# Optimization experiments

Measured on AMD Instinct MI355X. Metric: run time of the kernel, lower is better.

## Reference

```python
import jax, jax.numpy as jnp
import numpy as np

T, B, D, H, HH, OUT = 512, 128, 256, 1024, 256, 128
EPS = 1e-3

def _ln(x, gamma, beta):
    # layer_norm over feature dim, eps=0.001, matching torch reciprocal(sqrt(var+eps))
    m = jnp.mean(x, -1, keepdims=True)
    xs = x - m
    v = jnp.mean(xs * xs, -1, keepdims=True)
    return gamma * xs * jax.lax.rsqrt(v + EPS) + beta

def _ln_all(h, base, units, gamma, beta):
    # normalize each of `base` gate blocks independently over `units`
    b = h.shape[0]
    hr = h.reshape(b, base, units)
    m = jnp.mean(hr, -1, keepdims=True)
    xs = hr - m
    v = jnp.mean(xs * xs, -1, keepdims=True)
    hn = (xs * jax.lax.rsqrt(v + EPS)).reshape(b, base * units)
    return gamma * hn + beta

def setup_inputs() -> dict:
    key = jax.random.key(0)
    ks = jax.random.split(key, 12)
    return {
        "x": jax.random.normal(ks[0], (T, B, D), jnp.float32),
        "Wx": jax.random.normal(ks[1], (4 * H, D), jnp.float32) * (1.0 / np.sqrt(D)),
        "Wh": jax.random.normal(ks[2], (4 * H, H), jnp.float32) * (1.0 / np.sqrt(H)),
        "bias": jax.random.normal(ks[3], (4 * H,), jnp.float32) * 0.1,
        "lna_gamma": jnp.ones((4 * H,), jnp.float32),
        "lna_beta": jnp.zeros((4 * H,), jnp.float32),
        "ln_gamma": jnp.ones((H,), jnp.float32),
        "ln_beta": jnp.zeros((H,), jnp.float32),
        "zb": jax.random.normal(ks[4], (4, HH, HH), jnp.float32) * 0.01,   # ib/jb/fb/ob _zb
        "zbeta": jax.random.normal(ks[5], (4, HH, H), jnp.float32) * 0.01, # ib/jb/fb/ob _beta
        "zw_w": jax.random.normal(ks[6], (8, HH, HH), jnp.float32) * 0.01, # ix,jx,fx,ox,ih,jh,fh,oh _zw_w
        "zw_b": jnp.ones((8, HH), jnp.float32),
        "alpha": jnp.full((8, HH, H), 0.1 / HH, jnp.float32) + jax.random.normal(ks[7], (8, HH, H), jnp.float32) * 1e-4,
        "hyp_Wx": jax.random.normal(ks[8], (4 * HH, D + H), jnp.float32) * (1.0 / np.sqrt(D + H)),
        "hyp_bx": jnp.zeros((4 * HH,), jnp.float32),
        "hyp_Wh": jax.random.normal(ks[9], (4 * HH, HH), jnp.float32) * (1.0 / np.sqrt(HH)),
        "hyp_bh": jnp.zeros((4 * HH,), jnp.float32),
        "hyp_lna_gamma": jnp.ones((4 * HH,), jnp.float32),
        "hyp_lna_beta": jnp.zeros((4 * HH,), jnp.float32),
        "hyp_ln_gamma": jnp.ones((HH,), jnp.float32),
        "hyp_ln_beta": jnp.zeros((HH,), jnp.float32),
        "fc_W": jax.random.normal(ks[10], (OUT, H), jnp.float32) * (1.0 / np.sqrt(H)),
        "fc_b": jnp.zeros((OUT,), jnp.float32),
    }

def reference(x, Wx, Wh, bias, lna_gamma, lna_beta, ln_gamma, ln_beta, zb, zbeta,
              zw_w, zw_b, alpha, hyp_Wx, hyp_bx, hyp_Wh, hyp_bh,
              hyp_lna_gamma, hyp_lna_beta, hyp_ln_gamma, hyp_ln_beta, fc_W, fc_b):
    b4 = bias.reshape(4, H)

    def step(carry, xt):
        h, c, hh, ch = carry  # main (B,H), hyper (B,HH)
        # ---- hypernetwork LSTM cell (layer-norm LSTM) ----
        g = jnp.concatenate([xt, h], 1) @ hyp_Wx.T + hyp_bx + hh @ hyp_Wh.T + hyp_bh
        g = _ln_all(g, 4, HH, hyp_lna_gamma, hyp_lna_beta)
        hi, hf, hg, ho = jnp.split(g, 4, 1)  # ingate, forgetgate, cellgate, outgate
        ch_n = jax.nn.sigmoid(hf) * ch + jax.nn.sigmoid(hi) * jnp.tanh(hg)
        hyp = jax.nn.sigmoid(ho) * jnp.tanh(_ln(ch_n, hyp_ln_gamma, hyp_ln_beta))
        # ---- hyper-modulation: per-gate scale vectors and bias adjustments ----
        z = jnp.einsum('bq,kqp->kbp', hyp, zw_w) + zw_b[:, None, :]   # (8,B,HH)
        sc = jnp.einsum('kbp,kph->kbh', z, alpha)                     # (8,B,H)
        bz = jnp.einsum('bq,kqp->kbp', hyp, zb)                       # (4,B,HH)
        badj = jnp.einsum('kbp,kph->kbh', bz, zbeta)                  # (4,B,H)
        # ---- main LSTM gates (order i, j, f, o) ----
        xg = (xt @ Wx.T).reshape(B, 4, H).transpose(1, 0, 2)          # (4,B,H)
        hg2 = (h @ Wh.T).reshape(B, 4, H).transpose(1, 0, 2)          # (4,B,H)
        gates = sc[:4] * xg + sc[4:] * hg2 + b4[:, None, :] + badj    # (4,B,H)
        gates = _ln_all(gates.transpose(1, 0, 2).reshape(B, 4 * H), 4, H, lna_gamma, lna_beta)
        i, j, f, o = jnp.split(gates, 4, 1)
        c_n = jax.nn.sigmoid(f) * c + jax.nn.sigmoid(i) * jnp.tanh(j)
        h_n = jax.nn.sigmoid(o) * jnp.tanh(_ln(c_n, ln_gamma, ln_beta))
        return (h_n, c_n, hyp, ch_n), None

    init = (jnp.zeros((B, H), x.dtype), jnp.zeros((B, H), x.dtype),
            jnp.zeros((B, HH), x.dtype), jnp.zeros((B, HH), x.dtype))
    (h_f, _, _, _), _ = jax.lax.scan(step, init, x)
    return h_f @ fc_W.T + fc_b  # (B, OUT)
```

## Files before the change

### kernel.cpp

```cpp
#include <hip/hip_runtime.h>
#include <math.h>

#define T_STEPS 512
#define BATCH   128
#define DIN     256
#define HMAIN   1024
#define HHYP    256
#define OUTN    128
#define EPS     1e-3f

#define KSPLIT_NONE (1<<30)
#define NBLK 512

typedef __attribute__((ext_vector_type(4))) float f32x4;
typedef __attribute__((ext_vector_type(8))) short s16x8;

__device__ __forceinline__ float sigm(float x){ return 1.f/(1.f + expf(-x)); }

__device__ __forceinline__ unsigned short f2bf(float f){
    union { float f; unsigned u; } x; x.f = f;
    unsigned r = x.u + 0x7FFFu + ((x.u >> 16) & 1u);
    return (unsigned short)(r >> 16);
}

__device__ __forceinline__ float agf(const float* p){
    return __hip_atomic_load(const_cast<float*>(p), __ATOMIC_RELAXED, __HIP_MEMORY_SCOPE_AGENT);
}
__device__ __forceinline__ unsigned long long agu8(const void* p){
    return __hip_atomic_load(const_cast<unsigned long long*>((const unsigned long long*)p),
                             __ATOMIC_RELAXED, __HIP_MEMORY_SCOPE_AGENT);
}
__device__ __forceinline__ void agsf(float* p, float v){
    __hip_atomic_store(p, v, __ATOMIC_RELAXED, __HIP_MEMORY_SCOPE_AGENT);
}
__device__ __forceinline__ void agsu(unsigned* p, unsigned v){
    __hip_atomic_store(p, v, __ATOMIC_RELAXED, __HIP_MEMORY_SCOPE_AGENT);
}

__device__ __forceinline__ void gbar(unsigned* cnt, unsigned phase, int bid, int tid){
    __syncthreads();
    if (tid < 16){
        if (tid == (bid & 15))
            __hip_atomic_fetch_add(&cnt[tid*32], 1u, __ATOMIC_RELAXED, __HIP_MEMORY_SCOPE_AGENT);
        const unsigned tg = phase * (NBLK/16);
        while (__hip_atomic_load(&cnt[tid*32], __ATOMIC_RELAXED, __HIP_MEMORY_SCOPE_AGENT) < tg)
            __builtin_amdgcn_s_sleep(4);
    }
    __syncthreads();
}

#define BM 32
#define BN 64
#define KT 32
__device__ void gemm_dev(const float* __restrict__ A1, int lda1, int ksplit,
                         const float* __restrict__ A2, int lda2,
                         const float* __restrict__ Bp, int ldb, int b_nk,
                         const float* __restrict__ bias,
                         float* __restrict__ C, int ldc,
                         int K, int k0, int mtile, int ntile)
{
    __shared__ __align__(16) float As[KT][BM+4];
    __shared__ __align__(16) float Bs[KT][BN+4];
    const int tid = threadIdx.x;
    const int mt = tid >> 4, nt = tid & 15;
    const int m0g = mtile*BM, n0g = ntile*BN;
    float acc[4][4];
    #pragma unroll
    for (int i=0;i<4;++i) { acc[i][0]=0;acc[i][1]=0;acc[i][2]=0;acc[i][3]=0; }
    for (int kt = 0; kt < K; kt += KT) {
        __syncthreads();
        #pragma unroll
        for (int i=0;i<8;++i){
            int e = tid + i*128;
            int m = e >> 5, k = e & 31;
            int gk = k0 + kt + k, gm = m0g + m;
            float v = (gk < ksplit) ? A1[(size_t)gm*lda1 + gk]
                                    : A2[(size_t)gm*lda2 + (gk - ksplit)];
            As[k][m] = v;
        }
        if (b_nk) {
            #pragma unroll
            for (int i=0;i<16;++i){
                int e = tid + i*128;
                int n = e >> 5, k = e & 31;
                Bs[k][n] = Bp[(size_t)(n0g + n)*ldb + (k0 + kt + k)];
            }
        } else {
            #pragma unroll
            for (int i=0;i<16;++i){
                int e = tid + i*128;
                int k = e >> 6, n = e & 63;
                Bs[k][n] = Bp[(size_t)(k0 + kt + k)*ldb + (n0g + n)];
            }
        }
        __syncthreads();
        #pragma unroll
        for (int k=0;k<KT;++k){
            float4 av = *(const float4*)(&As[k][4*mt]);
            float4 bv = *(const float4*)(&Bs[k][4*nt]);
            acc[0][0]+=av.x*bv.x; acc[0][1]+=av.x*bv.y; acc[0][2]+=av.x*bv.z; acc[0][3]+=av.x*bv.w;
            acc[1][0]+=av.y*bv.x; acc[1][1]+=av.y*bv.y; acc[1][2]+=av.y*bv.z; acc[1][3]+=av.y*bv.w;
            acc[2][0]+=av.z*bv.x; acc[2][1]+=av.z*bv.y; acc[2][2]+=av.z*bv.z; acc[2][3]+=av.z*bv.w;
            acc[3][0]+=av.w*bv.x; acc[3][1]+=av.w*bv.y; acc[3][2]+=av.w*bv.z; acc[3][3]+=av.w*bv.w;
        }
    }
    #pragma unroll
    for (int i=0;i<4;++i){
        int gm = m0g + 4*mt + i;
        #pragma unroll
        for (int j=0;j<4;++j){
            int gn = n0g + 4*nt + j;
            float v = acc[i][j];
            if (bias) v += bias[gn];
            C[(size_t)gm*ldc + gn] = v;
        }
    }
}

#define ASTR 40
__device__ void gemm_mfma(const float* __restrict__ A1, int lda1, int ksplit,
                          const float* __restrict__ A2, int lda2,
                          const unsigned short* __restrict__ B, int ldb,
                          const float* __restrict__ bias,
                          float* __restrict__ C, int ldc,
                          int K, int k0, int mtile, int ntile)
{
    __shared__ __align__(16) unsigned short As[32*ASTR];
    __shared__ __align__(16) unsigned short Bs[128*ASTR];
    const int tid = threadIdx.x;
    const int lane = tid & 63, w = tid >> 6;
    const int wm = (w >> 1) * 16, wn = (w & 1) * 64;
    const int fr = lane & 15, koff = (lane >> 4) * 8;
    const int m0g = mtile*32, n0g = ntile*128;

    f32x4 acc[4];
    #pragma unroll
    for (int j=0;j<4;++j) acc[j] = (f32x4){0.f,0.f,0.f,0.f};

    const int arow = tid >> 3, akc = (tid & 7) * 4;
    for (int kt = 0; kt < K; kt += 32) {
        __syncthreads();
        {
            int gk = k0 + kt + akc;
            int gm = m0g + arow;
            const float* src = (gk < ksplit) ? (A1 + (size_t)gm*lda1 + gk)
                                             : (A2 + (size_t)gm*lda2 + (gk - ksplit));
            float4 v = *(const float4*)src;
            unsigned short* d = &As[arow*ASTR + akc];
            d[0] = f2bf(v.x); d[1] = f2bf(v.y); d[2] = f2bf(v.z); d[3] = f2bf(v.w);
        }
        #pragma unroll
        for (int i=0;i<4;++i){
            int e = tid + i*256;
            int n = e >> 3, kc = (e & 7) * 4;
            ushort4 bv = *(const ushort4*)(B + (size_t)(n0g + n)*ldb + (k0 + kt + kc));
            unsigned short* d = &Bs[n*ASTR + kc];
            d[0] = bv.x; d[1] = bv.y; d[2] = bv.z; d[3] = bv.w;
        }
        __syncthreads();
        s16x8 af = *(const s16x8*)&As[(wm + fr)*ASTR + koff];
        #pragma unroll
        for (int j=0;j<4;++j){
            s16x8 bf = *(const s16x8*)&Bs[(wn + j*16 + fr)*ASTR + koff];
            acc[j] = __builtin_amdgcn_mfma_f32_16x16x32_bf16(af, bf, acc[j], 0, 0, 0);
        }
    }
    #pragma unroll
    for (int j=0;j<4;++j){
        int gn = n0g + wn + j*16 + fr;
        float bb = bias ? bias[gn] : 0.f;
        #pragma unroll
        for (int r=0;r<4;++r){
            int gm = m0g + wm + (lane >> 4)*4 + r;
            C[(size_t)gm*ldc + gn] = acc[j][r] + bb;
        }
    }
}

#define WSTR 264
template<int NF, int AMODE>
__device__ __forceinline__ void gemm_ws(
    const void* __restrict__ Aptr, int lda,
    const unsigned short* wtile,
    const float* __restrict__ bias,
    float* __restrict__ Cout, int ldc,
    int lane, int w)
{
    const int fr = lane & 15, kq = lane >> 4;
    f32x4 acc[2][NF];
    #pragma unroll
    for (int mf=0; mf<2; ++mf)
        #pragma unroll
        for (int nf=0; nf<NF; ++nf) acc[mf][nf] = (f32x4){0.f,0.f,0.f,0.f};
    const int r0 = w*32 + fr;
    #pragma unroll
    for (int kt=0; kt<256; kt+=32) {
        const int k = kt + kq*8;
        s16x8 a[2];
        #pragma unroll
        for (int mf=0; mf<2; ++mf) {
            const int row = r0 + mf*16;
            if (AMODE == 0) {
                const float* s = (const float*)Aptr + (size_t)row*lda + k;
                float4 v0 = *(const float4*)s;
                float4 v1 = *(const float4*)(s+4);
                union { s16x8 v; unsigned short u[8]; } tc;
                tc.u[0]=f2bf(v0.x); tc.u[1]=f2bf(v0.y); tc.u[2]=f2bf(v0.z); tc.u[3]=f2bf(v0.w);
                tc.u[4]=f2bf(v1.x); tc.u[5]=f2bf(v1.y); tc.u[6]=f2bf(v1.z); tc.u[7]=f2bf(v1.w);
                a[mf] = tc.v;
            } else {
                const unsigned short* s = (const unsigned short*)Aptr + (size_t)row*lda + k;
                union { unsigned long long q[2]; s16x8 v; } tc;
                tc.q[0] = agu8(s);
                tc.q[1] = agu8(s + 4);
                a[mf] = tc.v;
            }
        }
        #pragma unroll
        for (int nf=0; nf<NF; ++nf) {
            s16x8 b = *(const s16x8*)&wtile[(nf*16+fr)*WSTR + k];
            acc[0][nf] = __builtin_amdgcn_mfma_f32_16x16x32_bf16(a[0], b, acc[0][nf], 0,0,0);
            acc[1][nf] = __builtin_amdgcn_mfma_f32_16x16x32_bf16(a[1], b, acc[1][nf], 0,0,0);
        }
    }
    #pragma unroll
    for (int nf=0; nf<NF; ++nf) {
        const int col = nf*16 + fr;
        const float bb = bias ? bias[col] : 0.f;
        #pragma unroll
        for (int mf=0; mf<2; ++mf) {
            const int row = w*32 + mf*16 + kq*4;
            #pragma unroll
            for (int r=0; r<4; ++r)
                agsf(&Cout[(size_t)(row+r)*ldc + col], acc[mf][nf][r] + bb);
        }
    }
}

__device__ __forceinline__ void load_wtile(const unsigned short* __restrict__ src,
                                           int ld, unsigned short* dst, int rows, int tid)
{
    const int chunks = rows * 32;
    for (int cidx = tid; cidx < chunks; cidx += 256) {
        const int r = cidx >> 5, k8 = (cidx & 31) << 3;
        *(uint4*)&dst[r*WSTR + k8] = *(const uint4*)&src[(size_t)r*ld + k8];
    }
}

__global__ __launch_bounds__(256) void k_prep_convert(
    const float* __restrict__ hyp_Wx, const float* __restrict__ hyp_Wh,
    const float* __restrict__ hyp_bx, const float* __restrict__ hyp_bh,
    const float* __restrict__ Wx, const float* __restrict__ Wh,
    unsigned short* __restrict__ wcat1bf, unsigned short* __restrict__ wxbf,
    unsigned short* __restrict__ whbf, float* __restrict__ bias1,
    float* __restrict__ act1f, float* __restrict__ c, float* __restrict__ ch,
    unsigned int* __restrict__ act1bf_zero, unsigned int* __restrict__ gcnt_zero)
{
    size_t i = (size_t)blockIdx.x*256 + threadIdx.x;
    if (i < 1572864u) {
        int n = (int)(i / 1536), k = (int)(i % 1536);
        float v = (k < 1280) ? hyp_Wx[(size_t)n*1280 + k] : hyp_Wh[(size_t)n*256 + (k-1280)];
        wcat1bf[i] = f2bf(v); return;
    }
    i -= 1572864u;
    if (i < 1048576u) { wxbf[i] = f2bf(Wx[i]); return; }
    i -= 1048576u;
    if (i < 4194304u) { whbf[i] = f2bf(Wh[i]); return; }
    i -= 4194304u;
    if (i < 1024u) { bias1[i] = hyp_bx[i] + hyp_bh[i]; return; }
    i -= 1024u;
    if (i < 163840u) { act1f[i] = 0.f; return; }
    i -= 163840u;
    if (i < 131072u) { c[i] = 0.f; return; }
    i -= 131072u;
    if (i < 32768u) { ch[i] = 0.f; return; }
    i -= 32768u;
    if (i < 81920u) { act1bf_zero[i] = 0u; return; }
    i -= 81920u;
    if (i < 512u) { gcnt_zero[i] = 0u; return; }
}
#define PREP_TOTAL 7226880u

__global__ __launch_bounds__(128) void k_prep_wcomb(
    const float* __restrict__ zw_w, const float* __restrict__ zb,
    const float* __restrict__ alpha, const float* __restrict__ zbeta,
    float* __restrict__ wcombf32)
{
    int kk = blockIdx.z;
    const float* A = (kk < 8) ? (zw_w + (size_t)kk*65536) : (zb + (size_t)(kk-8)*65536);
    const float* Bm = (kk < 8) ? (alpha + (size_t)kk*262144) : (zbeta + (size_t)(kk-8)*262144);
    gemm_dev(A, 256, KSPLIT_NONE, A, 256, Bm, 1024, 0, nullptr,
             wcombf32 + (size_t)kk*262144, 1024, 256, 0, blockIdx.x, blockIdx.y);
}

__global__ __launch_bounds__(256) void k_prep_cvtcomb(
    const float* __restrict__ wcombf32, unsigned short* __restrict__ wcombbf)
{
    size_t i = (size_t)blockIdx.x*256 + threadIdx.x;
    if (i >= 3145728u) return;
    int kk = (int)(i / 262144u);
    int r  = (int)(i % 262144u);
    int n = r / 256, k = r % 256;
    wcombbf[i] = f2bf(wcombf32[(size_t)kk*262144 + (size_t)k*1024 + n]);
}

__global__ __launch_bounds__(256) void k_prep_bcomb(
    const float* __restrict__ zw_b, const float* __restrict__ alpha,
    float* __restrict__ bcomb)
{
    int k = blockIdx.x;
    int n = blockIdx.y*256 + threadIdx.x;
    float s = 0.f;
    for (int p=0;p<256;++p)
        s += zw_b[k*256+p] * alpha[(size_t)k*262144 + (size_t)p*1024 + n];
    bcomb[(size_t)k*1024 + n] = s;
}

__device__ __forceinline__ void breduce2(float& a, float& b, volatile float* buf, int tid){
    #pragma unroll
    for (int off = 32; off > 0; off >>= 1) { a += __shfl_xor(a, off); b += __shfl_xor(b, off); }
    __syncthreads();
    if ((tid & 63) == 0) { buf[(tid>>6)*2] = a; buf[(tid>>6)*2+1] = b; }
    __syncthreads();
    a = buf[0] + buf[2] + buf[4] + buf[6];
    b = buf[1] + buf[3] + buf[5] + buf[7];
}

__device__ __forceinline__ void hyper_cell6(
    int b, int tid, volatile float* cbuf,
    const float* __restrict__ gpart, const float* __restrict__ bias1,
    const float* __restrict__ lna_g, const float* __restrict__ lna_b,
    const float* __restrict__ ln_g, const float* __restrict__ ln_b,
    float* __restrict__ ch, unsigned short* __restrict__ act1bf)
{
    float v[4];
    #pragma unroll
    for (int g=0; g<4; ++g){
        size_t idx = (size_t)b*1024 + g*256 + tid;
        v[g] = agf(&gpart[idx]) + agf(&gpart[131072+idx]) + agf(&gpart[262144+idx])
             + agf(&gpart[393216+idx]) + agf(&gpart[524288+idx]) + agf(&gpart[655360+idx])
             + bias1[g*256 + tid];
    }
    #pragma unroll
    for (int g=0; g<4; ++g){
        float s = v[g], ss = v[g]*v[g];
        breduce2(s, ss, cbuf, tid);
        float m = s * (1.f/256.f);
        float var = ss * (1.f/256.f) - m*m;
        v[g] = (v[g]-m)*rsqrtf(var + EPS)*lna_g[g*256+tid] + lna_b[g*256+tid];
    }
    float chp = ch[b*256 + tid];
    float cn = sigm(v[1])*chp + sigm(v[0])*tanhf(v[2]);
    float s = cn, ss = cn*cn;
    breduce2(s, ss, cbuf, tid);
    float m = s*(1.f/256.f);
    float var = ss*(1.f/256.f) - m*m;
    float hn = sigm(v[3]) * tanhf((cn-m)*rsqrtf(var + EPS)*ln_g[tid] + ln_b[tid]);
    ch[b*256 + tid] = cn;
    unsigned hb = f2bf(hn);
    unsigned other = __shfl_down(hb, 1);
    if (!(tid & 1))
        agsu((unsigned*)(act1bf + (size_t)b*1280 + 1024 + tid), hb | (other << 16));
}

__device__ __forceinline__ void main_cell2(
    int b, int tid, volatile float* cbuf,
    const float* __restrict__ bias4,
    const float* __restrict__ lna_g, const float* __restrict__ lna_b,
    const float* __restrict__ ln_g, const float* __restrict__ ln_b,
    const float* __restrict__ xgbuf, const float* __restrict__ hgpart,
    const float* __restrict__ scb,
    float* __restrict__ c, unsigned short* __restrict__ act1bf,
    float* __restrict__ hfc)
{
    float gn[4][4];
    #pragma unroll
    for (int k=0;k<4;++k){
        float pre[4]; float s=0.f, ss=0.f;
        #pragma unroll
        for (int j=0;j<4;++j){
            int h = j*256 + tid;
            int n = k*1024 + h;
            size_t bh = (size_t)b*1024 + h;
            size_t bn = (size_t)b*4096 + n;
            float xgv = agf(&xgbuf[bn]);
            float hgv = agf(&hgpart[bn]) + agf(&hgpart[524288+bn])
                      + agf(&hgpart[1048576+bn]) + agf(&hgpart[1572864+bn]);
            float p = agf(&scb[(size_t)k*131072 + bh])*xgv
                    + agf(&scb[(size_t)(4+k)*131072 + bh])*hgv
                    + bias4[n] + agf(&scb[(size_t)(8+k)*131072 + bh]);
            pre[j] = p; s += p; ss += p*p;
        }
        breduce2(s, ss, cbuf, tid);
        float m = s*(1.f/1024.f);
        float var = ss*(1.f/1024.f) - m*m;
        float rs = rsqrtf(var + EPS);
        #pragma unroll
        for (int j=0;j<4;++j){
            int h=j*256+tid, n=k*1024+h;
            gn[k][j] = (pre[j]-m)*rs*lna_g[n] + lna_b[n];
        }
    }
    float cnv[4]; float s=0.f, ss=0.f;
    #pragma unroll
    for (int j=0;j<4;++j){
        int h=j*256+tid;
        float cv = c[(size_t)b*1024+h];
        float x = sigm(gn[2][j])*cv + sigm(gn[0][j])*tanhf(gn[1][j]);
        cnv[j]=x; s+=x; ss+=x*x;
    }
    breduce2(s, ss, cbuf, tid);
    float m=s*(1.f/1024.f);
    float var=ss*(1.f/1024.f)-m*m;
    float rs=rsqrtf(var + EPS);
    #pragma unroll
    for (int j=0;j<4;++j){
        int h=j*256+tid;
        float hv = sigm(gn[3][j])*tanhf((cnv[j]-m)*rs*ln_g[h] + ln_b[h]);
        c[(size_t)b*1024+h] = cnv[j];
        hfc[(size_t)b*1024 + h] = hv;
        unsigned hb = f2bf(hv);
        unsigned other = __shfl_down(hb, 1);
        if (!(tid & 1))
            agsu((unsigned*)(act1bf + (size_t)b*1280 + h), hb | (other << 16));
    }
}

__device__ __forceinline__ void hyper_cell_body(
    const float* __restrict__ lna_g, const float* __restrict__ lna_b,
    const float* __restrict__ ln_g, const float* __restrict__ ln_b,
    const float* __restrict__ gpart, const float* __restrict__ bias1,
    float* __restrict__ ch, float* __restrict__ act1, int b, int tid)
{
    __shared__ float buf[8];
    float v[4];
    #pragma unroll
    for (int g=0; g<4; ++g){
        int idx = b*1024 + g*256 + tid;
        v[g] = gpart[idx] + gpart[131072 + idx] + gpart[262144 + idx] + gpart[393216 + idx]
             + bias1[g*256 + tid];
    }
    #pragma unroll
    for (int g=0; g<4; ++g){
        float s = v[g], ss = v[g]*v[g];
        breduce2(s, ss, buf, tid);
        float m = s * (1.f/256.f);
        float var = ss * (1.f/256.f) - m*m;
        v[g] = (v[g]-m)*rsqrtf(var + EPS)*lna_g[g*256+tid] + lna_b[g*256+tid];
    }
    float chp = ch[b*256 + tid];
    float cn = sigm(v[1])*chp + sigm(v[0])*tanhf(v[2]);
    float s = cn, ss = cn*cn;
    breduce2(s, ss, buf, tid);
    float m = s*(1.f/256.f);
    float var = ss*(1.f/256.f) - m*m;
    float hn = sigm(v[3]) * tanhf((cn-m)*rsqrtf(var + EPS)*ln_g[tid] + ln_b[tid]);
    ch[b*256 + tid] = cn;
    act1[b*1280 + 1024 + tid] = hn;
}

__device__ __forceinline__ void main_cell_body(
    const float* __restrict__ bias4,
    const float* __restrict__ lna_g, const float* __restrict__ lna_b,
    const float* __restrict__ ln_g, const float* __restrict__ ln_b,
    const float* __restrict__ xghg, const float* __restrict__ scb,
    float* __restrict__ c, float* __restrict__ act1, int b, int tid)
{
    __shared__ float buf[8];
    float gn[4][4];
    #pragma unroll
    for (int k=0;k<4;++k){
        float pre[4]; float s=0.f, ss=0.f;
        #pragma unroll
        for (int j=0;j<4;++j){
            int h = j*256 + tid;
            int n = k*1024 + h;
            int bh = b*1024 + h;
            float xgv = xghg[b*4096 + n];
            float hgv = xghg[524288 + b*4096 + n];
            float p = scb[k*131072 + bh]*xgv + scb[(4+k)*131072 + bh]*hgv
                    + bias4[n] + scb[(8+k)*131072 + bh];
            pre[j] = p; s += p; ss += p*p;
        }
        breduce2(s, ss, buf, tid);
        float m = s*(1.f/1024.f);
        float var = ss*(1.f/1024.f) - m*m;
        float rs = rsqrtf(var + EPS);
        #pragma unroll
        for (int j=0;j<4;++j){
            int h=j*256+tid, n=k*1024+h;
            gn[k][j] = (pre[j]-m)*rs*lna_g[n] + lna_b[n];
        }
    }
    float cnv[4]; float s=0.f, ss=0.f;
    #pragma unroll
    for (int j=0;j<4;++j){
        int h=j*256+tid;
        float cv = c[b*1024+h];
        float x = sigm(gn[2][j])*cv + sigm(gn[0][j])*tanhf(gn[1][j]);
        cnv[j]=x; s+=x; ss+=x*x;
    }
    breduce2(s, ss, buf, tid);
    float m=s*(1.f/1024.f);
    float var=ss*(1.f/1024.f)-m*m;
    float rs=rsqrtf(var + EPS);
    #pragma unroll
    for (int j=0;j<4;++j){
        int h=j*256+tid;
        float hv = sigm(gn[3][j])*tanhf((cnv[j]-m)*rs*ln_g[h] + ln_b[h]);
        c[b*1024+h] = cnv[j];
        act1[b*1280 + h] = hv;
    }
}

__global__ __launch_bounds__(256) void k_step1(
    const float* __restrict__ xt, const float* __restrict__ act1,
    const unsigned short* __restrict__ wcat1bf,
    const unsigned short* __restrict__ wxbf, const unsigned short* __restrict__ whbf,
    float* __restrict__ gpart, float* __restrict__ xghg)
{
    int bid = blockIdx.x;
    if (bid < 128) {
        int sp = bid >> 5, r = bid & 31;
        gemm_mfma(xt, 256, 256, act1, 1280, wcat1bf, 1536, nullptr,
                  gpart + (size_t)sp*131072, 1024, 384, sp*384, r >> 3, r & 7);
    } else if (bid < 256) {
        int r = bid - 128;
        gemm_mfma(xt, 256, KSPLIT_NONE, xt, 256, wxbf, 256, nullptr,
                  xghg, 4096, 256, 0, r >> 5, r & 31);
    } else {
        int r = bid - 256;
        gemm_mfma(act1, 1280, KSPLIT_NONE, act1, 1280, whbf, 1024, nullptr,
                  xghg + 524288, 4096, 1024, 0, r >> 5, r & 31);
    }
}

__global__ __launch_bounds__(256) void k_step2(
    const float* __restrict__ act1, const unsigned short* __restrict__ wcombbf,
    const float* __restrict__ bcomb, float* __restrict__ scb)
{
    int bid = blockIdx.x;
    int kk = bid >> 5, r = bid & 31;
    const float* bias = (kk < 8) ? (bcomb + (size_t)kk*1024) : nullptr;
    gemm_mfma(act1 + 1024, 1280, KSPLIT_NONE, act1 + 1024, 1280,
              wcombbf + (size_t)kk*262144, 256, bias,
              scb + (size_t)kk*131072, 1024, 256, 0, r >> 3, r & 7);
}

__global__ __launch_bounds__(256) void k_hyper_cell(
    const float* __restrict__ lna_g, const float* __restrict__ lna_b,
    const float* __restrict__ ln_g, const float* __restrict__ ln_b,
    const float* __restrict__ gpart, const float* __restrict__ bias1,
    float* __restrict__ ch, float* __restrict__ act1)
{
    hyper_cell_body(lna_g, lna_b, ln_g, ln_b, gpart, bias1, ch, act1,
                    blockIdx.x, threadIdx.x);
}

__global__ __launch_bounds__(256) void k_main_cell(
    const float* __restrict__ bias4,
    const float* __restrict__ lna_g, const float* __restrict__ lna_b,
    const float* __restrict__ ln_g, const float* __restrict__ ln_b,
    const float* __restrict__ xghg, const float* __restrict__ scb,
    float* __restrict__ c, float* __restrict__ act1)
{
    main_cell_body(bias4, lna_g, lna_b, ln_g, ln_b, xghg, scb, c, act1,
                   blockIdx.x, threadIdx.x);
}

__global__ __launch_bounds__(256, 2) void k_persist4(
    const float* __restrict__ x,
    const unsigned short* __restrict__ wcat1bf,
    const unsigned short* __restrict__ wxbf,
    const unsigned short* __restrict__ whbf,
    const unsigned short* __restrict__ wcombbf,
    const float* __restrict__ bcomb, const float* __restrict__ bias1,
    const float* __restrict__ bias4,
    const float* __restrict__ lna_g, const float* __restrict__ lna_b,
    const float* __restrict__ ln_g, const float* __restrict__ ln_b,
    const float* __restrict__ hlna_g, const float* __restrict__ hlna_b,
    const float* __restrict__ hln_g, const float* __restrict__ hln_b,
    float* __restrict__ gpart, float* __restrict__ hgpart,
    float* __restrict__ xgbuf, float* __restrict__ scb,
    unsigned short* __restrict__ act1bf, float* __restrict__ hfc,
    float* __restrict__ c, float* __restrict__ ch,
    unsigned* __restrict__ gcnt)
{
    const int bid = blockIdx.x, tid = threadIdx.x;
    const int lane = tid & 63, w = tid >> 6;
    __shared__ __align__(16) unsigned short wlds[25344];
    __shared__ float cbuf[8];

    if (bid < 96) {
        load_wtile(wcat1bf + (size_t)((bid & 15)*64)*1536 + (bid >> 4)*256,
                   1536, wlds, 64, tid);
    } else if (bid < 352) {
        int h_ = bid - 96;
        load_wtile(whbf + (size_t)((h_ >> 2)*64)*1024 + (h_ & 3)*256,
                   1024, wlds, 64, tid);
    } else if (bid < 416) {
        load_wtile(wxbf + (size_t)(bid - 352)*64*256, 256, wlds, 64, tid);
    }
    if (bid < 384) {
        int kk = bid >> 5, mt = bid & 31;
        load_wtile(wcombbf + (size_t)kk*262144 + (size_t)(mt*32)*256,
                   256, wlds + 16896, 32, tid);
    }
    __syncthreads();

    unsigned phase = 0;
    for (int t = 0; t < T_STEPS; ++t) {
        const float* xt = x + (size_t)t*BATCH*DIN;

        if (bid < 96) {
            int nt = bid & 15, sp = bid >> 4;
            float* outp = gpart + (size_t)sp*131072 + nt*64;
            if (sp == 0)
                gemm_ws<4,0>(xt, 256, wlds, nullptr, outp, 1024, lane, w);
            else
                gemm_ws<4,2>(act1bf + (sp-1)*256, 1280, wlds, nullptr, outp, 1024, lane, w);
        }
        gbar(gcnt, ++phase, bid, tid);

        if (bid >= 96 && bid < 352) {
            int h_ = bid - 96, nt = h_ >> 2, sp = h_ & 3;
            gemm_ws<4,2>(act1bf + sp*256, 1280, wlds, nullptr,
                         hgpart + (size_t)sp*524288 + nt*64, 4096, lane, w);
        } else if (bid >= 352 && bid < 416) {
            gemm_ws<4,0>(xt, 256, wlds, nullptr,
                         xgbuf + (bid - 352)*64, 4096, lane, w);
        } else {
            int row = (bid >= 416) ? (bid - 416) : (bid < 32 ? 96 + bid : -1);
            if (row >= 0)
                hyper_cell6(row, tid, cbuf, gpart, bias1,
                            hlna_g, hlna_b, hln_g, hln_b, ch, act1bf);
        }
        gbar(gcnt, ++phase, bid, tid);

        if (bid < 384) {
            int kk = bid >> 5, mt = bid & 31;
            const float* bp = (kk < 8) ? (bcomb + (size_t)kk*1024 + mt*32) : nullptr;
            gemm_ws<2,2>(act1bf + 1024, 1280, wlds + 16896, bp,
                         scb + (size_t)kk*131072 + mt*32, 1024, lane, w);
        }
        gbar(gcnt, ++phase, bid, tid);

        if (bid < 128)
            main_cell2(bid, tid, cbuf, bias4, lna_g, lna_b, ln_g, ln_b,
                       xgbuf, hgpart, scb, c, act1bf, hfc);
        gbar(gcnt, ++phase, bid, tid);
    }
}

__global__ __launch_bounds__(128) void k_fc2(
    const float* __restrict__ fcW, const float* __restrict__ fcb,
    const float* __restrict__ hsrc, int ldh, float* __restrict__ out)
{
    int b = blockIdx.x, o = threadIdx.x;
    const float* h = hsrc + (size_t)b*ldh;
    float s = fcb[o];
    for (int k=0;k<1024;++k) s += h[k]*fcW[(size_t)o*1024 + k];
    out[b*OUTN + o] = s;
}

extern "C" void kernel_launch(void* const* d_in, const int* in_sizes, int n_in,
                              void* d_out, int out_size, void* d_ws, size_t ws_size,
                              hipStream_t stream)
{
    const float* x        = (const float*)d_in[0];
    const float* Wx       = (const float*)d_in[1];
    const float* Wh       = (const float*)d_in[2];
    const float* bias     = (const float*)d_in[3];
    const float* lna_g    = (const float*)d_in[4];
    const float* lna_b    = (const float*)d_in[5];
    const float* ln_g     = (const float*)d_in[6];
    const float* ln_b     = (const float*)d_in[7];
    const float* zb       = (const float*)d_in[8];
    const float* zbeta    = (const float*)d_in[9];
    const float* zw_w     = (const float*)d_in[10];
    const float* zw_b     = (const float*)d_in[11];
    const float* alpha    = (const float*)d_in[12];
    const float* hyp_Wx   = (const float*)d_in[13];
    const float* hyp_bx   = (const float*)d_in[14];
    const float* hyp_Wh   = (const float*)d_in[15];
    const float* hyp_bh   = (const float*)d_in[16];
    const float* hlna_g   = (const float*)d_in[17];
    const float* hlna_b   = (const float*)d_in[18];
    const float* hln_g    = (const float*)d_in[19];
    const float* hln_b    = (const float*)d_in[20];
    const float* fcW      = (const float*)d_in[21];
    const float* fcb      = (const float*)d_in[22];
    float* out = (float*)d_out;

    unsigned short* wcat1bf = (unsigned short*)d_ws;
    unsigned short* wxbf    = wcat1bf + 1572864;
    unsigned short* whbf    = wxbf + 1048576;
    unsigned short* wcombbf = whbf + 4194304;
    unsigned short* act1bf  = wcombbf + 3145728;
    float* fbase = (float*)(act1bf + 163840);
    float* bcomb = fbase;
    float* bias1 = bcomb + 8192;
    float* hfc   = bias1 + 1024;
    float* c     = hfc + 131072;
    float* ch    = c + 131072;
    float* act1o = ch + 32768;
    float* gpart = act1o + 163840;
    float* hgpart= gpart + 786432;
    float* xgbuf = hgpart + 2097152;
    float* scb   = xgbuf + 524288;
    unsigned* gcnt = (unsigned*)(scb + 1572864);
    float* wcombf32 = gpart;

    k_prep_convert<<<(PREP_TOTAL + 255)/256, 256, 0, stream>>>(
        hyp_Wx, hyp_Wh, hyp_bx, hyp_bh, Wx, Wh,
        wcat1bf, wxbf, whbf, bias1, act1o, c, ch,
        (unsigned int*)act1bf, gcnt);
    k_prep_wcomb<<<dim3(8,16,12), 128, 0, stream>>>(zw_w, zb, alpha, zbeta, wcombf32);
    k_prep_bcomb<<<dim3(8,4), 256, 0, stream>>>(zw_b, alpha, bcomb);
    k_prep_cvtcomb<<<(3145728 + 255)/256, 256, 0, stream>>>(wcombf32, wcombbf);

    static int use_pers = -1;
    if (use_pers < 0) {
        use_pers = 0;
        int dev = 0;
        if (hipGetDevice(&dev) == hipSuccess) {
            hipDeviceProp_t prop;
            if (hipGetDeviceProperties(&prop, dev) == hipSuccess) {
                int occ = 0;
                if (hipOccupancyMaxActiveBlocksPerMultiprocessor(
                        &occ, (const void*)k_persist4, 256, 0) == hipSuccess &&
                    occ >= 2 && occ * prop.multiProcessorCount >= NBLK) {
                    use_pers = 1;
                }
            }
        }
    }

    if (use_pers) {
        k_persist4<<<NBLK, 256, 0, stream>>>(
            x, wcat1bf, wxbf, whbf, wcombbf,
            bcomb, bias1, bias,
            lna_g, lna_b, ln_g, ln_b,
            hlna_g, hlna_b, hln_g, hln_b,
            gpart, hgpart, xgbuf, scb,
            act1bf, hfc, c, ch, gcnt);
        k_fc2<<<BATCH, 128, 0, stream>>>(fcW, fcb, hfc, 1024, out);
        return;
    }

    float* xghg = hgpart;
    for (int t = 0; t < T_STEPS; ++t) {
        const float* xt = x + (size_t)t*BATCH*DIN;
        k_step1<<<384, 256, 0, stream>>>(xt, act1o, wcat1bf, wxbf, whbf, gpart, xghg);
        k_hyper_cell<<<BATCH, 256, 0, stream>>>(hlna_g, hlna_b, hln_g, hln_b,
                                                gpart, bias1, ch, act1o);
        k_step2<<<384, 256, 0, stream>>>(act1o, wcombbf, bcomb, scb);
        k_main_cell<<<BATCH, 256, 0, stream>>>(bias, lna_g, lna_b, ln_g, ln_b,
                                               xghg, scb, c, act1o);
    }
    k_fc2<<<BATCH, 128, 0, stream>>>(fcW, fcb, act1o, 1280, out);
}
```

Measured before the change: 34.07 ms.

## Use a master-broadcast grid barrier and run hgpart/xg GEMMs in the first phase

Replaces the distributed 16-counter grid barrier with a two-level scheme. Every block increments a sharded counter, block 0 waits for all shards, then publishes the phase in a single flag that all other blocks poll with one thread. The Wh-hidden and Wx-input GEMMs now run in the same phase as the hyper-GEMM, so the phase with the hyper cell only does the hyper cell. The aim is to cut polling contention and barrier latency, and to shorten the critical path of each timestep. The cost is an extra hop through block 0 at every barrier, plus a bigger counter buffer to zero.

Measured after the change: 34.15 ms. Within noise of the previous version (+0.2%).

```diff
diff --git a/kernel.cpp b/kernel.cpp
--- a/kernel.cpp
+++ b/kernel.cpp
@@ -36,15 +36,29 @@
 __device__ __forceinline__ void agsu(unsigned* p, unsigned v){
     __hip_atomic_store(p, v, __ATOMIC_RELAXED, __HIP_MEMORY_SCOPE_AGENT);
 }
+__device__ __forceinline__ unsigned aglu(const unsigned* p){
+    return __hip_atomic_load(const_cast<unsigned*>(p), __ATOMIC_RELAXED, __HIP_MEMORY_SCOPE_AGENT);
+}
 
 __device__ __forceinline__ void gbar(unsigned* cnt, unsigned phase, int bid, int tid){
     __syncthreads();
-    if (tid < 16){
-        if (tid == (bid & 15))
-            __hip_atomic_fetch_add(&cnt[tid*32], 1u, __ATOMIC_RELAXED, __HIP_MEMORY_SCOPE_AGENT);
-        const unsigned tg = phase * (NBLK/16);
-        while (__hip_atomic_load(&cnt[tid*32], __ATOMIC_RELAXED, __HIP_MEMORY_SCOPE_AGENT) < tg)
-            __builtin_amdgcn_s_sleep(4);
+    if (bid == 0) {
+        if (tid < 16) {
+            if (tid == 0)
+                __hip_atomic_fetch_add(&cnt[0], 1u, __ATOMIC_RELAXED, __HIP_MEMORY_SCOPE_AGENT);
+            const unsigned tg = phase * (NBLK/16);
+            while (aglu(&cnt[tid*32]) < tg)
+                __builtin_amdgcn_s_sleep(1);
+        }
+        __syncthreads();
+        if (tid == 0)
+            agsu(&cnt[512], phase);
+    } else {
+        if (tid == 0) {
+            __hip_atomic_fetch_add(&cnt[(bid & 15)*32], 1u, __ATOMIC_RELAXED, __HIP_MEMORY_SCOPE_AGENT);
+            while (aglu(&cnt[512]) < phase)
+                __builtin_amdgcn_s_sleep(4);
+        }
     }
     __syncthreads();
 }
@@ -277,9 +291,9 @@
     i -= 32768u;
     if (i < 81920u) { act1bf_zero[i] = 0u; return; }
     i -= 81920u;
-    if (i < 512u) { gcnt_zero[i] = 0u; return; }
-}
-#define PREP_TOTAL 7226880u
+    if (i < 1024u) { gcnt_zero[i] = 0u; return; }
+}
+#define PREP_TOTAL 7227392u
 
 __global__ __launch_bounds__(128) void k_prep_wcomb(
     const float* __restrict__ zw_w, const float* __restrict__ zb,
@@ -568,7 +582,7 @@
                    blockIdx.x, threadIdx.x);
 }
 
-__global__ __launch_bounds__(256, 2) void k_persist4(
+__global__ __launch_bounds__(256, 2) void k_persist5(
     const float* __restrict__ x,
     const unsigned short* __restrict__ wcat1bf,
     const unsigned short* __restrict__ wxbf,
@@ -619,17 +633,17 @@
                 gemm_ws<4,0>(xt, 256, wlds, nullptr, outp, 1024, lane, w);
             else
                 gemm_ws<4,2>(act1bf + (sp-1)*256, 1280, wlds, nullptr, outp, 1024, lane, w);
-        }
-        gbar(gcnt, ++phase, bid, tid);
-
-        if (bid >= 96 && bid < 352) {
+        } else if (bid < 352) {
             int h_ = bid - 96, nt = h_ >> 2, sp = h_ & 3;
             gemm_ws<4,2>(act1bf + sp*256, 1280, wlds, nullptr,
                          hgpart + (size_t)sp*524288 + nt*64, 4096, lane, w);
-        } else if (bid >= 352 && bid < 416) {
+        } else if (bid < 416) {
             gemm_ws<4,0>(xt, 256, wlds, nullptr,
                          xgbuf + (bid - 352)*64, 4096, lane, w);
-        } else {
+        }
+        gbar(gcnt, ++phase, bid, tid);
+
+        {
             int row = (bid >= 416) ? (bid - 416) : (bid < 32 ? 96 + bid : -1);
             if (row >= 0)
                 hyper_cell6(row, tid, cbuf, gpart, bias1,
@@ -728,7 +742,7 @@
             if (hipGetDeviceProperties(&prop, dev) == hipSuccess) {
                 int occ = 0;
                 if (hipOccupancyMaxActiveBlocksPerMultiprocessor(
-                        &occ, (const void*)k_persist4, 256, 0) == hipSuccess &&
+                        &occ, (const void*)k_persist5, 256, 0) == hipSuccess &&
                     occ >= 2 && occ * prop.multiProcessorCount >= NBLK) {
                     use_pers = 1;
                 }
@@ -737,7 +751,7 @@
     }
 
     if (use_pers) {
-        k_persist4<<<NBLK, 256, 0, stream>>>(
+        k_persist5<<<NBLK, 256, 0, stream>>>(
             x, wcat1bf, wxbf, whbf, wcombbf,
             bcomb, bias1, bias,
             lna_g, lna_b, ln_g, ln_b,
```
